# Kernel optimization log

Hardware: AMD Instinct MI355X
Metric: run time of the kernel (lower is better)

The kernel has to match this reference:

```python
import jax, jax.numpy as jnp
import numpy as np

DIM = 2048
H = 16
QLR = 1536
KVLR = 512
NOPE = 128
ROPE = 64
VH = 128
QKH = NOPE + ROPE  # 192
B, S = 2, 2048
EPS = 1e-6


def _rmsnorm(x, w):
    return x * jax.lax.rsqrt(jnp.mean(x * x, axis=-1, keepdims=True) + EPS) * w


def _rope_cos_sin(seq_len, r, dtype):
    inv_freq = 1.0 / (10000.0 ** (jnp.arange(0, r, 2, dtype=jnp.float32) / r))
    ang = jnp.arange(seq_len, dtype=jnp.float32)[:, None] * inv_freq  # [S, r/2]
    return jnp.cos(ang).astype(dtype), jnp.sin(ang).astype(dtype)


def _rot(t, cos, sin):
    # rotate-half RoPE on last dim; cos/sin pre-broadcast to t's rank
    t1, t2 = jnp.split(t, 2, axis=-1)
    return jnp.concatenate([t1 * cos - t2 * sin, t2 * cos + t1 * sin], axis=-1)


def setup_inputs() -> dict:
    key = jax.random.key(0)
    ks = jax.random.split(key, 12)
    sd = 0.02
    return {
        "x": jax.random.normal(ks[0], (B, S, DIM), jnp.float32),
        "wqd": jax.random.normal(ks[1], (DIM, QLR), jnp.float32) * sd,
        "bqd": jnp.zeros((QLR,), jnp.float32),
        "qnorm_w": jnp.ones((QLR,), jnp.float32),
        "wqu": jax.random.normal(ks[2], (QLR, H * QKH), jnp.float32) * sd,
        "bqu": jnp.zeros((H * QKH,), jnp.float32),
        "wkvd": jax.random.normal(ks[3], (DIM, KVLR + ROPE), jnp.float32) * sd,
        "bkvd": jnp.zeros((KVLR + ROPE,), jnp.float32),
        "kvnorm_w": jnp.ones((KVLR,), jnp.float32),
        "wkvu": jax.random.normal(ks[4], (KVLR, H * (NOPE + VH)), jnp.float32) * sd,
        "bkvu": jnp.zeros((H * (NOPE + VH),), jnp.float32),
        "wout": jax.random.normal(ks[5], (H * VH, DIM), jnp.float32) * sd,
        "bout": jnp.zeros((DIM,), jnp.float32),
    }


def reference(x, wqd, bqd, qnorm_w, wqu, bqu, wkvd, bkvd, kvnorm_w, wkvu, bkvu, wout, bout):
    b, s, _ = x.shape
    # Q path: low-rank down, RMSNorm, up; split nope / rope
    q = _rmsnorm(x @ wqd + bqd, qnorm_w) @ wqu + bqu        # [b,s,H*QKH]
    q = q.reshape(b, s, H, QKH)
    q_nope, q_rope = q[..., :NOPE], q[..., NOPE:]
    # KV path: joint down-proj -> kv latent + shared rope key
    kvd = x @ wkvd + bkvd                                   # [b,s,KVLR+ROPE]
    kv_lora, k_rope = kvd[..., :KVLR], kvd[..., KVLR:]
    cos, sin = _rope_cos_sin(s, ROPE, x.dtype)
    q_rope = _rot(q_rope, cos[None, :, None, :], sin[None, :, None, :])
    k_rope = _rot(k_rope, cos[None, :, :], sin[None, :, :])  # [b,s,ROPE]
    kvu = _rmsnorm(kv_lora, kvnorm_w) @ wkvu + bkvu          # [b,s,H*(NOPE+VH)]
    kvu = kvu.reshape(b, s, H, NOPE + VH)
    k_nope, v = kvu[..., :NOPE], kvu[..., NOPE:]
    k_rope_b = jnp.broadcast_to(k_rope[:, :, None, :], (b, s, H, ROPE))
    qf = jnp.concatenate([q_nope, q_rope], axis=-1)          # [b,s,H,QKH]
    kf = jnp.concatenate([k_nope, k_rope_b], axis=-1)        # [b,s,H,QKH]
    scale = QKH ** -0.5
    scores = jnp.einsum('bqhd,bkhd->bhqk', qf, kf) * scale
    causal = jnp.tril(jnp.ones((s, s), bool))
    scores = jnp.where(causal, scores, jnp.finfo(scores.dtype).min)
    attn = jax.nn.softmax(scores, axis=-1)
    o = jnp.einsum('bhqk,bkhd->bqhd', attn, v).reshape(b, s, H * VH)
    return o @ wout + bout
```

## Files before the change

kernel.cpp:

```cpp
#include <hip/hip_runtime.h>
#include <hip/hip_bf16.h>
#include <math.h>

#define HH 16
#define SS 2048
#define BBATCH 2
#define NROWS 4096

typedef __attribute__((ext_vector_type(8))) __bf16 bf16x8;
typedef __attribute__((ext_vector_type(4))) float f32x4;
typedef const __attribute__((address_space(1))) unsigned int* gas1_t;
typedef __attribute__((address_space(3))) unsigned int* las3_t;

__device__ __forceinline__ unsigned short f2bf(float f) {
  unsigned u = __builtin_bit_cast(unsigned, f);
  u += 0x7fffu + ((u >> 16) & 1u);
  return (unsigned short)(u >> 16);
}

__device__ __forceinline__ void gload16(const void* g, void* l) {
  __builtin_amdgcn_global_load_lds((gas1_t)g, (las3_t)l, 16, 0, 0);
}
__device__ __forceinline__ f32x4 mfma16(bf16x8 a, bf16x8 b, f32x4 c) {
  return __builtin_amdgcn_mfma_f32_16x16x32_bf16(a, b, c, 0, 0, 0);
}

__global__ __launch_bounds__(256) void k_convert(const float* __restrict__ in,
                                                 unsigned short* __restrict__ out, long n4) {
  long i = (long)blockIdx.x * blockDim.x + threadIdx.x;
  long stride = (long)gridDim.x * blockDim.x;
  for (; i < n4; i += stride) {
    float4 v = ((const float4*)in)[i];
    ushort4 o = { f2bf(v.x), f2bf(v.y), f2bf(v.z), f2bf(v.w) };
    ((ushort4*)out)[i] = o;
  }
}

__global__ __launch_bounds__(256) void k_transpose(const float* __restrict__ W,
                                                   unsigned short* __restrict__ Wt,
                                                   int K, int N, int Npad) {
  __shared__ float tile[32][33];
  int n0 = blockIdx.x * 32, k0 = blockIdx.y * 32;
  int tx = threadIdx.x & 31, ty = threadIdx.x >> 5;
  for (int i = ty; i < 32; i += 8) {
    int k = k0 + i, n = n0 + tx;
    tile[i][tx] = (k < K && n < N) ? W[(long)k * N + n] : 0.f;
  }
  __syncthreads();
  for (int i = ty; i < 32; i += 8) {
    int n = n0 + i, k = k0 + tx;
    if (n < Npad && k < K) Wt[(long)n * K + k] = f2bf(tile[tx][i]);
  }
}

__global__ __launch_bounds__(256) void k_bias_merge(const float* __restrict__ bqd,
                                                    const float* __restrict__ bkvd,
                                                    float* __restrict__ mb) {
  int i = blockIdx.x * 256 + threadIdx.x;
  if (i < 2176) mb[i] = i < 1536 ? bqd[i] : (i < 2112 ? bkvd[i - 1536] : 0.f);
}

__global__ __launch_bounds__(64) void k_rope_table(float2* __restrict__ tab) {
  int s = blockIdx.x * 2 + (threadIdx.x >> 5);
  int i = threadIdx.x & 31;
  float inv = powf(10000.f, -(float)i / 32.f);
  float ang = (float)s * inv;
  float sn, cs;
  sincosf(ang, &sn, &cs);
  tab[s * 32 + i] = make_float2(cs, sn);
}

__global__ __launch_bounds__(256) void k_gemm(const unsigned short* __restrict__ A,
                                              const unsigned short* __restrict__ Bt,
                                              const float* __restrict__ bias,
                                              float* __restrict__ C,
                                              int M, int N, int K) {
  __shared__ unsigned short lA[128 * 32];
  __shared__ unsigned short lB[128 * 32];
  int tid = threadIdx.x;
  int wave = tid >> 6, lane = tid & 63;
  int l15 = lane & 15, lhi = lane >> 4;
  int ntn = (N + 127) >> 7;
  int tm = blockIdx.x / ntn, tn = blockIdx.x % ntn;
  long row0 = (long)tm * 128, col0 = (long)tn * 128;
  int wr = wave >> 1, wc = wave & 1;

  const unsigned short* gA = A + (row0 + (tid >> 2)) * K + (tid & 3) * 8;
  const unsigned short* gB = Bt + (col0 + (tid >> 2)) * K + (tid & 3) * 8;
  unsigned short* lA0 = &lA[tid * 8];
  unsigned short* lB0 = &lB[tid * 8];

  f32x4 acc[4][4] = {};
  for (int k0 = 0; k0 < K; k0 += 32) {
    __syncthreads();
    gload16(gA + k0, lA0);
    gload16(gA + (long)64 * K + k0, lA0 + 2048);
    gload16(gB + k0, lB0);
    gload16(gB + (long)64 * K + k0, lB0 + 2048);
    asm volatile("s_waitcnt vmcnt(0)" ::: "memory");
    __syncthreads();
    bf16x8 af[4], bfr[4];
#pragma unroll
    for (int i = 0; i < 4; ++i) {
      af[i]  = *(const bf16x8*)&lA[(wr * 64 + i * 16 + l15) * 32 + lhi * 8];
      bfr[i] = *(const bf16x8*)&lB[(wc * 64 + i * 16 + l15) * 32 + lhi * 8];
    }
#pragma unroll
    for (int i = 0; i < 4; ++i)
#pragma unroll
      for (int j = 0; j < 4; ++j)
        acc[i][j] = mfma16(af[i], bfr[j], acc[i][j]);
  }
#pragma unroll
  for (int i = 0; i < 4; ++i)
#pragma unroll
    for (int j = 0; j < 4; ++j) {
      long r = row0 + wr * 64 + i * 16 + lhi * 4;
      long c = col0 + wc * 64 + j * 16 + l15;
      if (c < N) {
        float bv = bias[c];
#pragma unroll
        for (int rr = 0; rr < 4; ++rr)
          C[(r + rr) * N + c] = acc[i][j][rr] + bv;
      }
    }
}

__global__ __launch_bounds__(256) void k_gemm_qf(const unsigned short* __restrict__ A,
                                                 const unsigned short* __restrict__ Bt,
                                                 const float* __restrict__ bias,
                                                 const float2* __restrict__ rtab,
                                                 unsigned short* __restrict__ qf,
                                                 int M, int N, int K) {
  __shared__ unsigned short lA[128 * 32];
  __shared__ unsigned short lB[128 * 32];
  int tid = threadIdx.x;
  int wave = tid >> 6, lane = tid & 63;
  int l15 = lane & 15, lhi = lane >> 4;
  int ntn = (N + 127) >> 7;
  int tm = blockIdx.x / ntn, tn = blockIdx.x % ntn;
  long row0 = (long)tm * 128, col0 = (long)tn * 128;
  int wr = wave >> 1, wc = wave & 1;

  const unsigned short* gA = A + (row0 + (tid >> 2)) * K + (tid & 3) * 8;
  const unsigned short* gB = Bt + (col0 + (tid >> 2)) * K + (tid & 3) * 8;
  unsigned short* lA0 = &lA[tid * 8];
  unsigned short* lB0 = &lB[tid * 8];

  f32x4 acc[4][4] = {};
  for (int k0 = 0; k0 < K; k0 += 32) {
    __syncthreads();
    gload16(gA + k0, lA0);
    gload16(gA + (long)64 * K + k0, lA0 + 2048);
    gload16(gB + k0, lB0);
    gload16(gB + (long)64 * K + k0, lB0 + 2048);
    asm volatile("s_waitcnt vmcnt(0)" ::: "memory");
    __syncthreads();
    bf16x8 af[4], bfr[4];
#pragma unroll
    for (int i = 0; i < 4; ++i) {
      af[i]  = *(const bf16x8*)&lA[(wr * 64 + i * 16 + l15) * 32 + lhi * 8];
      bfr[i] = *(const bf16x8*)&lB[(wc * 64 + i * 16 + l15) * 32 + lhi * 8];
    }
#pragma unroll
    for (int i = 0; i < 4; ++i)
#pragma unroll
      for (int j = 0; j < 4; ++j)
        acc[i][j] = mfma16(af[i], bfr[j], acc[i][j]);
  }

  const float scq = 0.07216878364870322f * 1.4426950408889634f;
  int base = (int)col0 + wc * 64;
  int h = base / 192;
  int m192 = base - h * 192;
  float bv[4];
#pragma unroll
  for (int j = 0; j < 4; ++j) bv[j] = bias[base + j * 16 + l15];

#pragma unroll
  for (int i = 0; i < 4; ++i) {
#pragma unroll
    for (int rr = 0; rr < 4; ++rr) {
      long r = row0 + wr * 64 + i * 16 + lhi * 4 + rr;
      int s = (int)(r & 2047), b = (int)(r >> 11);
      unsigned short* dst = qf + (((long)(b * HH + h)) * SS + s) * 192;
      if (m192 < 128) {
#pragma unroll
        for (int j = 0; j < 4; ++j)
          dst[m192 + j * 16 + l15] = f2bf((acc[i][j][rr] + bv[j]) * scq);
      } else {
#pragma unroll
        for (int j = 0; j < 2; ++j) {
          int ifq = j * 16 + l15;
          float2 cs = rtab[s * 32 + ifq];
          float v1 = acc[i][j][rr] + bv[j];
          float v2 = acc[i][j + 2][rr] + bv[j + 2];
          dst[128 + ifq] = f2bf((v1 * cs.x - v2 * cs.y) * scq);
          dst[160 + ifq] = f2bf((v2 * cs.x + v1 * cs.y) * scq);
        }
      }
    }
  }
}

__global__ __launch_bounds__(256) void k_gemm_kv(const unsigned short* __restrict__ A,
                                                 const unsigned short* __restrict__ Bt,
                                                 const float* __restrict__ bias,
                                                 unsigned short* __restrict__ kf3,
                                                 unsigned short* __restrict__ vt3,
                                                 int M, int N, int K) {
  __shared__ unsigned short smem[16384];
  unsigned short* lA = smem;
  unsigned short* lB = smem + 4096;
  int tid = threadIdx.x;
  int wave = tid >> 6, lane = tid & 63;
  int l15 = lane & 15, lhi = lane >> 4;
  int ntn = N >> 7;
  int tm = blockIdx.x / ntn, tn = blockIdx.x % ntn;
  long row0 = (long)tm * 128, col0 = (long)tn * 128;
  int wr = wave >> 1, wc = wave & 1;

  const unsigned short* gA = A + (row0 + (tid >> 2)) * K + (tid & 3) * 8;
  const unsigned short* gB = Bt + (col0 + (tid >> 2)) * K + (tid & 3) * 8;
  unsigned short* lA0 = &lA[tid * 8];
  unsigned short* lB0 = &lB[tid * 8];

  f32x4 acc[4][4] = {};
  for (int k0 = 0; k0 < K; k0 += 32) {
    __syncthreads();
    gload16(gA + k0, lA0);
    gload16(gA + (long)64 * K + k0, lA0 + 2048);
    gload16(gB + k0, lB0);
    gload16(gB + (long)64 * K + k0, lB0 + 2048);
    asm volatile("s_waitcnt vmcnt(0)" ::: "memory");
    __syncthreads();
    bf16x8 af[4], bfr[4];
#pragma unroll
    for (int i = 0; i < 4; ++i) {
      af[i]  = *(const bf16x8*)&lA[(wr * 64 + i * 16 + l15) * 32 + lhi * 8];
      bfr[i] = *(const bf16x8*)&lB[(wc * 64 + i * 16 + l15) * 32 + lhi * 8];
    }
#pragma unroll
    for (int i = 0; i < 4; ++i)
#pragma unroll
      for (int j = 0; j < 4; ++j)
        acc[i][j] = mfma16(af[i], bfr[j], acc[i][j]);
  }

  int base = (int)col0 + wc * 64;
  int h = base >> 8;
  bool isv = (base & 255) >= 128;
  float bv[4];
#pragma unroll
  for (int j = 0; j < 4; ++j) bv[j] = bias[base + j * 16 + l15];

  int b = (int)(row0 >> 11);
  long bh = (long)b * HH + h;
  int lrb = wr * 64;
  __syncthreads();

  if (isv) {
#pragma unroll
    for (int i = 0; i < 4; ++i) {
      int lr = lrb + i * 16 + lhi * 4;
#pragma unroll
      for (int j = 0; j < 4; ++j) {
        int lc = wc * 64 + j * 16 + l15;
        ushort4 pk = { f2bf(acc[i][j][0] + bv[j]), f2bf(acc[i][j][1] + bv[j]),
                       f2bf(acc[i][j][2] + bv[j]), f2bf(acc[i][j][3] + bv[j]) };
        *(ushort4*)&smem[((lr >> 5) << 12) + lc * 32 + (lr & 31)] = pk;
      }
    }
    __syncthreads();
    long dst0 = (bh * 64 + ((row0 & 2047) >> 5)) * 4096;
#pragma unroll
    for (int p = 0; p < 8; ++p) {
      int e = p * 256 + tid;
      *(uint4*)&vt3[dst0 + e * 8] = *(uint4*)&smem[e * 8];
    }
  } else {
#pragma unroll
    for (int i = 0; i < 4; ++i) {
      int lr0 = lrb + i * 16 + lhi * 4;
#pragma unroll
      for (int j = 0; j < 4; ++j) {
        int c = (base & 255) + j * 16 + l15;
        int tbase = ((lr0 >> 4) << 11) + ((c >> 5) << 9) + (((c >> 3) & 3) << 7) + (c & 7);
#pragma unroll
        for (int rr = 0; rr < 4; ++rr)
          smem[tbase + ((lr0 + rr) & 15) * 8] = f2bf(acc[i][j][rr] + bv[j]);
      }
    }
    __syncthreads();
    long kb3 = (bh * 128 + ((row0 & 2047) >> 4)) * 3072;
#pragma unroll
    for (int p = 0; p < 8; ++p) {
      int e = p * 256 + tid;
      int tile = e >> 6;
      int off = (e & 63) * 8;
      long dst = kb3 + ((long)(tile >> 2) * 6 + (tile & 3)) * 512 + off;
      *(uint4*)&kf3[dst] = *(uint4*)&smem[tile * 512 + off];
    }
  }
}

__global__ __launch_bounds__(256) void k_rmsnorm(const float* __restrict__ X,
                                                 const float* __restrict__ w,
                                                 unsigned short* __restrict__ Y,
                                                 int L, int ldx) {
  long row = blockIdx.x;
  const float* x = X + row * ldx;
  float ss = 0.f;
  int n4 = L >> 2;
  for (int i = threadIdx.x; i < n4; i += 256) {
    float4 v = ((const float4*)x)[i];
    ss += v.x * v.x + v.y * v.y + v.z * v.z + v.w * v.w;
  }
  for (int off = 32; off > 0; off >>= 1) ss += __shfl_xor(ss, off);
  __shared__ float sb[4];
  if ((threadIdx.x & 63) == 0) sb[threadIdx.x >> 6] = ss;
  __syncthreads();
  float scale = rsqrtf((sb[0] + sb[1] + sb[2] + sb[3]) / (float)L + 1e-6f);
  unsigned short* y = Y + row * L;
  for (int i = threadIdx.x; i < L; i += 256)
    y[i] = f2bf(x[i] * scale * w[i]);
}

__global__ __launch_bounds__(64) void k_extract_krope(const float* __restrict__ sC,
                                                      unsigned short* __restrict__ kf3) {
  int bs = blockIdx.x;
  int lane = threadIdx.x;
  int s = bs & (SS - 1), b = bs >> 11;
  const float* src = sC + (long)bs * 2176 + 2048;
  int i = lane & 31;
  float inv = powf(10000.f, -(float)i / 32.f);
  float ang = (float)s * inv;
  float sn, cs;
  sincosf(ang, &sn, &cs);
  float t1 = src[i], t2 = src[32 + i];
  float v = (lane < 32) ? (t1 * cs - t2 * sn) : (t2 * cs + t1 * sn);
  unsigned short bv = f2bf(v);
  int d = 128 + lane;
  long inner = (long)(d >> 5) * 512 + ((d >> 3) & 3) * 128 + (s & 15) * 8 + (d & 7);
#pragma unroll
  for (int h = 0; h < HH; ++h) {
    long blk = ((long)(b * HH + h) * 128 + (s >> 4)) * 6;
    kf3[blk * 512 + inner] = bv;
  }
}

__global__ __launch_bounds__(256, 4) void k_attn(const unsigned short* __restrict__ qf,
                                                 const unsigned short* __restrict__ kf3,
                                                 const unsigned short* __restrict__ vt3,
                                                 unsigned short* __restrict__ o,
                                                 float* __restrict__ pO,
                                                 float* __restrict__ pml) {
  __shared__ unsigned short kbuf[64 * 192];
  __shared__ unsigned short pbuf[4][16 * 72];
  int tid = threadIdx.x;
  int wave = tid >> 6, lane = tid & 63;
  int l15 = lane & 15, lhi = lane >> 4;
  int idx = blockIdx.x;
  int rp = idx >> 5, bh = idx & 31;
  int qt, t0, t1, item;
  bool dodiag;
  if (rp < 48) {
    qt = 31 - (rp >> 1);
    int part = rp & 1;
    int h0 = (qt + 1) >> 1;
    t0 = part ? h0 : 0;
    t1 = part ? qt + 1 : h0;
    item = (bh * 24 + (qt - 8)) * 2 + part;
    dodiag = (part == 1);
  } else {
    qt = 55 - rp;
    t0 = 0;
    t1 = qt + 1;
    item = -1;
    dodiag = true;
  }
  int b = bh >> 4, h = bh & 15;
  int q0 = qt * 64;
  const char* kbase = (const char*)(kf3 + (long)bh * 128 * 3072);
  const unsigned short* vfrag0 = vt3 + (long)bh * 64 * 4096 + l15 * 32 + lhi * 8;
  const unsigned short* kread = kbuf + lane * 8;

  {
    const char* src = kbase + (long)t0 * 24576 + tid * 16;
    char* dst = (char*)kbuf + tid * 16;
#pragma unroll
    for (int p = 0; p < 6; ++p) gload16(src + p * 4096, dst + p * 4096);
  }

  const unsigned short* Qb = qf + ((long)bh * SS + q0 + wave * 16 + l15) * 192 + lhi * 8;
  bf16x8 qfr[6];
#pragma unroll
  for (int ks = 0; ks < 6; ++ks) qfr[ks] = *(const bf16x8*)(Qb + ks * 32);

  float m = -3e38f, ls = 0.f;
  f32x4 acc[8] = {};
  int qin = wave * 16 + l15;

  for (int t = t0; t < t1; ++t) {
    asm volatile("s_waitcnt vmcnt(0)" ::: "memory");
    __builtin_amdgcn_s_barrier();
    __builtin_amdgcn_sched_barrier(0);

    f32x4 sc[4] = {};
    __builtin_amdgcn_s_setprio(1);
#pragma unroll
    for (int ks = 0; ks < 6; ++ks) {
      bf16x8 kfr[4];
#pragma unroll
      for (int nf = 0; nf < 4; ++nf)
        kfr[nf] = *(const bf16x8*)&kread[(nf * 6 + ks) * 512];
#pragma unroll
      for (int nf = 0; nf < 4; ++nf)
        sc[nf] = mfma16(kfr[nf], qfr[ks], sc[nf]);
    }
    __builtin_amdgcn_s_setprio(0);
    __builtin_amdgcn_sched_barrier(0);
    __builtin_amdgcn_s_barrier();
    __builtin_amdgcn_sched_barrier(0);

    const unsigned short* vtb = vfrag0 + (long)t * 8192;
    bf16x8 v0[8];
#pragma unroll
    for (int nf = 0; nf < 8; ++nf) v0[nf] = *(const bf16x8*)(vtb + nf * 512);
    __builtin_amdgcn_sched_barrier(0);

    if (t + 1 < t1) {
      const char* src = kbase + (long)(t + 1) * 24576 + tid * 16;
      char* dst = (char*)kbuf + tid * 16;
#pragma unroll
      for (int p = 0; p < 6; ++p) gload16(src + p * 4096, dst + p * 4096);
    }

    bool diag = dodiag && (t == t1 - 1);
    float mnf[4];
#pragma unroll
    for (int nf = 0; nf < 4; ++nf) {
      if (diag) {
#pragma unroll
        for (int jj = 0; jj < 4; ++jj) {
          int kin = nf * 16 + lhi * 4 + jj;
          if (kin > qin) sc[nf][jj] = -3e38f;
        }
      }
      mnf[nf] = fmaxf(fmaxf(sc[nf][0], sc[nf][1]), fmaxf(sc[nf][2], sc[nf][3]));
    }
    float mx = fmaxf(fmaxf(mnf[0], mnf[1]), fmaxf(mnf[2], mnf[3]));
    mx = fmaxf(mx, __shfl_xor(mx, 16));
    mx = fmaxf(mx, __shfl_xor(mx, 32));
    if (!__all(mx <= m + 8.f)) {
      float mn = fmaxf(m, mx);
      float alpha = exp2f(m - mn);
      m = mn;
      ls *= alpha;
#pragma unroll
      for (int nf = 0; nf < 8; ++nf)
#pragma unroll
        for (int jj = 0; jj < 4; ++jj) acc[nf][jj] *= alpha;
    }
    float pnf[4];
#pragma unroll
    for (int nf = 0; nf < 4; ++nf) {
      float e0 = exp2f(sc[nf][0] - m), e1 = exp2f(sc[nf][1] - m);
      float e2 = exp2f(sc[nf][2] - m), e3 = exp2f(sc[nf][3] - m);
      pnf[nf] = (e0 + e1) + (e2 + e3);
      ushort4 pk = { f2bf(e0), f2bf(e1), f2bf(e2), f2bf(e3) };
      *(ushort4*)&pbuf[wave][l15 * 72 + nf * 16 + lhi * 4] = pk;
    }
    float ps = (pnf[0] + pnf[1]) + (pnf[2] + pnf[3]);
    ps += __shfl_xor(ps, 16);
    ps += __shfl_xor(ps, 32);
    ls += ps;

    {
      bf16x8 pf = *(const bf16x8*)&pbuf[wave][l15 * 72 + lhi * 8];
      __builtin_amdgcn_s_setprio(1);
#pragma unroll
      for (int nf = 0; nf < 8; ++nf) acc[nf] = mfma16(v0[nf], pf, acc[nf]);
      __builtin_amdgcn_s_setprio(0);
    }
    bf16x8 v1[8];
#pragma unroll
    for (int nf = 0; nf < 8; ++nf) v1[nf] = *(const bf16x8*)(vtb + 4096 + nf * 512);
    {
      bf16x8 pf = *(const bf16x8*)&pbuf[wave][l15 * 72 + 32 + lhi * 8];
      __builtin_amdgcn_s_setprio(1);
#pragma unroll
      for (int nf = 0; nf < 8; ++nf) acc[nf] = mfma16(v1[nf], pf, acc[nf]);
      __builtin_amdgcn_s_setprio(0);
    }
  }

  int qloc = wave * 16 + l15;
  if (item < 0) {
    float invl = 1.f / ls;
    long orow = (long)b * SS + q0 + qloc;
#pragma unroll
    for (int nf = 0; nf < 8; ++nf) {
      ushort4 ov = { f2bf(acc[nf][0] * invl), f2bf(acc[nf][1] * invl),
                     f2bf(acc[nf][2] * invl), f2bf(acc[nf][3] * invl) };
      *(ushort4*)&o[orow * 2048 + h * 128 + nf * 16 + lhi * 4] = ov;
    }
  } else {
    float* po = pO + (long)item * 8192 + qloc * 128;
#pragma unroll
    for (int nf = 0; nf < 8; ++nf)
      *(float4*)&po[nf * 16 + lhi * 4] = __builtin_bit_cast(float4, acc[nf]);
    if (lhi == 0) {
      pml[(long)item * 128 + qloc * 2] = m;
      pml[(long)item * 128 + qloc * 2 + 1] = ls;
    }
  }
}

__global__ __launch_bounds__(256) void k_merge(const float* __restrict__ pO,
                                               const float* __restrict__ pml,
                                               unsigned short* __restrict__ o) {
  int item2 = blockIdx.x;
  int bh = item2 / 24, qt = (item2 % 24) + 8;
  int b = bh >> 4, h = bh & 15;
  int q0 = qt * 64;
  long i0 = (long)item2 * 2, i1 = i0 + 1;
  __shared__ float w0s[64], w1s[64];
  int tid = threadIdx.x;
  if (tid < 64) {
    float m0 = pml[i0 * 128 + tid * 2], ls0 = pml[i0 * 128 + tid * 2 + 1];
    float m1 = pml[i1 * 128 + tid * 2], ls1 = pml[i1 * 128 + tid * 2 + 1];
    float mm = fmaxf(m0, m1);
    float w0 = exp2f(m0 - mm), w1 = exp2f(m1 - mm);
    float inv = 1.f / (ls0 * w0 + ls1 * w1);
    w0s[tid] = w0 * inv;
    w1s[tid] = w1 * inv;
  }
  __syncthreads();
  const float* p0 = pO + i0 * 8192;
  const float* p1 = pO + i1 * 8192;
#pragma unroll
  for (int p = 0; p < 8; ++p) {
    int e = p * 256 + tid;
    int q = e >> 5, d4 = (e & 31) * 4;
    float4 a = *(const float4*)&p0[q * 128 + d4];
    float4 c = *(const float4*)&p1[q * 128 + d4];
    float w0 = w0s[q], w1 = w1s[q];
    ushort4 ov = { f2bf(a.x * w0 + c.x * w1), f2bf(a.y * w0 + c.y * w1),
                   f2bf(a.z * w0 + c.z * w1), f2bf(a.w * w0 + c.w * w1) };
    *(ushort4*)&o[((long)b * SS + q0 + q) * 2048 + h * 128 + d4] = ov;
  }
}

extern "C" void kernel_launch(void* const* d_in, const int* in_sizes, int n_in,
                              void* d_out, int out_size, void* d_ws, size_t ws_size,
                              hipStream_t stream) {
  const float* x    = (const float*)d_in[0];
  const float* wqd  = (const float*)d_in[1];
  const float* bqd  = (const float*)d_in[2];
  const float* qnw  = (const float*)d_in[3];
  const float* wqu  = (const float*)d_in[4];
  const float* bqu  = (const float*)d_in[5];
  const float* wkvd = (const float*)d_in[6];
  const float* bkvd = (const float*)d_in[7];
  const float* kvnw = (const float*)d_in[8];
  const float* wkvu = (const float*)d_in[9];
  const float* bkvu = (const float*)d_in[10];
  const float* wout = (const float*)d_in[11];
  const float* bout = (const float*)d_in[12];
  float* out = (float*)d_out;

  char* ws = (char*)d_ws;
  size_t off = 0;
  auto alloc = [&](size_t sz) {
    char* p = ws + off;
    off += (sz + 255) & ~(size_t)255;
    return p;
  };
  unsigned short* xb    = (unsigned short*)alloc((size_t)NROWS * 2048 * 2);
  unsigned short* wqkt  = (unsigned short*)alloc((size_t)2176 * 2048 * 2);
  unsigned short* wqut  = (unsigned short*)alloc((size_t)3072 * 1536 * 2);
  unsigned short* wkvut = (unsigned short*)alloc((size_t)4096 * 512 * 2);
  unsigned short* woutt = (unsigned short*)alloc((size_t)2048 * 2048 * 2);
  unsigned short* qn    = (unsigned short*)alloc((size_t)NROWS * 1536 * 2);
  unsigned short* kvn   = (unsigned short*)alloc((size_t)NROWS * 512 * 2);
  unsigned short* qfb   = (unsigned short*)alloc((size_t)32 * SS * 192 * 2);
  unsigned short* kfb   = (unsigned short*)alloc((size_t)32 * SS * 192 * 2);
  unsigned short* vtb   = (unsigned short*)alloc((size_t)32 * 128 * SS * 2);
  unsigned short* ob    = (unsigned short*)alloc((size_t)NROWS * 2048 * 2);
  float*  mbias = (float*)alloc((size_t)2176 * 4);
  float2* rtab  = (float2*)alloc((size_t)SS * 32 * 8);
  float*  pO    = (float*)alloc((size_t)32 * 24 * 2 * 8192 * 4);
  float*  pml   = (float*)alloc((size_t)32 * 24 * 2 * 128 * 4);
  float* sC = (float*)alloc((size_t)NROWS * 2176 * 4);

  k_convert<<<2048, 256, 0, stream>>>(x, xb, (long)NROWS * 2048 / 4);
  k_transpose<<<dim3(48, 64), 256, 0, stream>>>(wqd, wqkt, 2048, 1536, 1536);
  k_transpose<<<dim3(20, 64), 256, 0, stream>>>(wkvd, wqkt + (size_t)1536 * 2048, 2048, 576, 640);
  k_transpose<<<dim3(96, 48), 256, 0, stream>>>(wqu, wqut, 1536, 3072, 3072);
  k_transpose<<<dim3(128, 16), 256, 0, stream>>>(wkvu, wkvut, 512, 4096, 4096);
  k_transpose<<<dim3(64, 64), 256, 0, stream>>>(wout, woutt, 2048, 2048, 2048);
  k_bias_merge<<<9, 256, 0, stream>>>(bqd, bkvd, mbias);
  k_rope_table<<<SS / 2, 64, 0, stream>>>(rtab);

  k_gemm<<<32 * 17, 256, 0, stream>>>(xb, wqkt, mbias, sC, NROWS, 2176, 2048);

  k_rmsnorm<<<NROWS, 256, 0, stream>>>(sC, qnw, qn, 1536, 2176);
  k_gemm_qf<<<32 * 24, 256, 0, stream>>>(qn, wqut, bqu, rtab, qfb, NROWS, 3072, 1536);

  k_rmsnorm<<<NROWS, 256, 0, stream>>>(sC + 1536, kvnw, kvn, 512, 2176);
  k_extract_krope<<<NROWS, 64, 0, stream>>>(sC, kfb);
  k_gemm_kv<<<32 * 32, 256, 0, stream>>>(kvn, wkvut, bkvu, kfb, vtb, NROWS, 4096, 512);

  k_attn<<<1792, 256, 0, stream>>>(qfb, kfb, vtb, ob, pO, pml);
  k_merge<<<768, 256, 0, stream>>>(pO, pml, ob);

  k_gemm<<<32 * 16, 256, 0, stream>>>(ob, woutt, bout, out, NROWS, 2048, 2048);
}
```

Before: 415.0 us.

## Split long causal attention rows into up to four KV parts; store down-proj in bf16

The attention work split changes from at most two KV chunks per query tile to two, three or four chunks depending on causal length, giving 2560 blocks in place of 1792. The merge kernel now combines up to four partial results with log-sum-exp weights. The goal is better load balance and fewer long tail blocks. Separately, the first down-projection GEMM now writes bf16 instead of fp32, which halves the traffic read by rmsnorm and the k_rope extract, at the cost of rounding the pre-norm activations to bf16.

```diff
diff --git a/kernel.cpp b/kernel.cpp
--- a/kernel.cpp
+++ b/kernel.cpp
@@ -16,6 +16,9 @@
   unsigned u = __builtin_bit_cast(unsigned, f);
   u += 0x7fffu + ((u >> 16) & 1u);
   return (unsigned short)(u >> 16);
+}
+__device__ __forceinline__ float bf2f(unsigned short u) {
+  return __builtin_bit_cast(float, (unsigned)u << 16);
 }
 
 __device__ __forceinline__ void gload16(const void* g, void* l) {
@@ -122,6 +125,62 @@
 #pragma unroll
         for (int rr = 0; rr < 4; ++rr)
           C[(r + rr) * N + c] = acc[i][j][rr] + bv;
+      }
+    }
+}
+
+__global__ __launch_bounds__(256) void k_gemm_c16(const unsigned short* __restrict__ A,
+                                                  const unsigned short* __restrict__ Bt,
+                                                  const float* __restrict__ bias,
+                                                  unsigned short* __restrict__ C,
+                                                  int M, int N, int K) {
+  __shared__ unsigned short lA[128 * 32];
+  __shared__ unsigned short lB[128 * 32];
+  int tid = threadIdx.x;
+  int wave = tid >> 6, lane = tid & 63;
+  int l15 = lane & 15, lhi = lane >> 4;
+  int ntn = (N + 127) >> 7;
+  int tm = blockIdx.x / ntn, tn = blockIdx.x % ntn;
+  long row0 = (long)tm * 128, col0 = (long)tn * 128;
+  int wr = wave >> 1, wc = wave & 1;
+
+  const unsigned short* gA = A + (row0 + (tid >> 2)) * K + (tid & 3) * 8;
+  const unsigned short* gB = Bt + (col0 + (tid >> 2)) * K + (tid & 3) * 8;
+  unsigned short* lA0 = &lA[tid * 8];
+  unsigned short* lB0 = &lB[tid * 8];
+
+  f32x4 acc[4][4] = {};
+  for (int k0 = 0; k0 < K; k0 += 32) {
+    __syncthreads();
+    gload16(gA + k0, lA0);
+    gload16(gA + (long)64 * K + k0, lA0 + 2048);
+    gload16(gB + k0, lB0);
+    gload16(gB + (long)64 * K + k0, lB0 + 2048);
+    asm volatile("s_waitcnt vmcnt(0)" ::: "memory");
+    __syncthreads();
+    bf16x8 af[4], bfr[4];
+#pragma unroll
+    for (int i = 0; i < 4; ++i) {
+      af[i]  = *(const bf16x8*)&lA[(wr * 64 + i * 16 + l15) * 32 + lhi * 8];
+      bfr[i] = *(const bf16x8*)&lB[(wc * 64 + i * 16 + l15) * 32 + lhi * 8];
+    }
+#pragma unroll
+    for (int i = 0; i < 4; ++i)
+#pragma unroll
+      for (int j = 0; j < 4; ++j)
+        acc[i][j] = mfma16(af[i], bfr[j], acc[i][j]);
+  }
+#pragma unroll
+  for (int i = 0; i < 4; ++i)
+#pragma unroll
+    for (int j = 0; j < 4; ++j) {
+      long r = row0 + wr * 64 + i * 16 + lhi * 4;
+      long c = col0 + wc * 64 + j * 16 + l15;
+      if (c < N) {
+        float bv = bias[c];
+#pragma unroll
+        for (int rr = 0; rr < 4; ++rr)
+          C[(r + rr) * N + c] = f2bf(acc[i][j][rr] + bv);
       }
     }
 }
@@ -304,17 +363,18 @@
   }
 }
 
-__global__ __launch_bounds__(256) void k_rmsnorm(const float* __restrict__ X,
+__global__ __launch_bounds__(256) void k_rmsnorm(const unsigned short* __restrict__ X,
                                                  const float* __restrict__ w,
                                                  unsigned short* __restrict__ Y,
                                                  int L, int ldx) {
   long row = blockIdx.x;
-  const float* x = X + row * ldx;
+  const unsigned short* x = X + row * ldx;
   float ss = 0.f;
   int n4 = L >> 2;
   for (int i = threadIdx.x; i < n4; i += 256) {
-    float4 v = ((const float4*)x)[i];
-    ss += v.x * v.x + v.y * v.y + v.z * v.z + v.w * v.w;
+    ushort4 v = ((const ushort4*)x)[i];
+    float a = bf2f(v.x), bb = bf2f(v.y), c = bf2f(v.z), d = bf2f(v.w);
+    ss += a * a + bb * bb + c * c + d * d;
   }
   for (int off = 32; off > 0; off >>= 1) ss += __shfl_xor(ss, off);
   __shared__ float sb[4];
@@ -323,21 +383,21 @@
   float scale = rsqrtf((sb[0] + sb[1] + sb[2] + sb[3]) / (float)L + 1e-6f);
   unsigned short* y = Y + row * L;
   for (int i = threadIdx.x; i < L; i += 256)
-    y[i] = f2bf(x[i] * scale * w[i]);
-}
-
-__global__ __launch_bounds__(64) void k_extract_krope(const float* __restrict__ sC,
+    y[i] = f2bf(bf2f(x[i]) * scale * w[i]);
+}
+
+__global__ __launch_bounds__(64) void k_extract_krope(const unsigned short* __restrict__ sC,
                                                       unsigned short* __restrict__ kf3) {
   int bs = blockIdx.x;
   int lane = threadIdx.x;
   int s = bs & (SS - 1), b = bs >> 11;
-  const float* src = sC + (long)bs * 2176 + 2048;
+  const unsigned short* src = sC + (long)bs * 2176 + 2048;
   int i = lane & 31;
   float inv = powf(10000.f, -(float)i / 32.f);
   float ang = (float)s * inv;
   float sn, cs;
   sincosf(ang, &sn, &cs);
-  float t1 = src[i], t2 = src[32 + i];
+  float t1 = bf2f(src[i]), t2 = bf2f(src[32 + i]);
   float v = (lane < 32) ? (t1 * cs - t2 * sn) : (t2 * cs + t1 * sn);
   unsigned short bv = f2bf(v);
   int d = 128 + lane;
@@ -362,22 +422,19 @@
   int l15 = lane & 15, lhi = lane >> 4;
   int idx = blockIdx.x;
   int rp = idx >> 5, bh = idx & 31;
-  int qt, t0, t1, item;
-  bool dodiag;
-  if (rp < 48) {
-    qt = 31 - (rp >> 1);
-    int part = rp & 1;
-    int h0 = (qt + 1) >> 1;
-    t0 = part ? h0 : 0;
-    t1 = part ? qt + 1 : h0;
-    item = (bh * 24 + (qt - 8)) * 2 + part;
-    dodiag = (part == 1);
-  } else {
-    qt = 55 - rp;
-    t0 = 0;
-    t1 = qt + 1;
-    item = -1;
-    dodiag = true;
+  int qt, part, np;
+  if (rp < 32)      { qt = 24 + (rp >> 2); part = rp & 3; np = 4; }
+  else if (rp < 56) { int r = rp - 32; qt = 16 + r / 3; part = r % 3; np = 3; }
+  else if (rp < 72) { int r = rp - 56; qt = 8 + (r >> 1); part = r & 1; np = 2; }
+  else              { qt = 79 - rp; part = 0; np = 1; }
+  int nt = qt + 1;
+  int t0 = nt * part / np, t1 = nt * (part + 1) / np;
+  bool dodiag = (part == np - 1);
+  int item;
+  if (np == 1) item = -1;
+  else {
+    int base = (qt < 16) ? (qt - 8) * 2 : (qt < 24) ? 16 + (qt - 16) * 3 : 40 + (qt - 24) * 4;
+    item = bh * 72 + base + part;
   }
   int b = bh >> 4, h = bh & 15;
   int q0 = qt * 64;
@@ -520,34 +577,45 @@
 __global__ __launch_bounds__(256) void k_merge(const float* __restrict__ pO,
                                                const float* __restrict__ pml,
                                                unsigned short* __restrict__ o) {
-  int item2 = blockIdx.x;
-  int bh = item2 / 24, qt = (item2 % 24) + 8;
+  int g = blockIdx.x;
+  int bh = g / 24, qt = (g % 24) + 8;
   int b = bh >> 4, h = bh & 15;
   int q0 = qt * 64;
-  long i0 = (long)item2 * 2, i1 = i0 + 1;
-  __shared__ float w0s[64], w1s[64];
+  int np = qt < 16 ? 2 : (qt < 24 ? 3 : 4);
+  int base = (qt < 16) ? (qt - 8) * 2 : (qt < 24) ? 16 + (qt - 16) * 3 : 40 + (qt - 24) * 4;
+  long i0 = (long)bh * 72 + base;
+  __shared__ float wts[4][64];
   int tid = threadIdx.x;
   if (tid < 64) {
-    float m0 = pml[i0 * 128 + tid * 2], ls0 = pml[i0 * 128 + tid * 2 + 1];
-    float m1 = pml[i1 * 128 + tid * 2], ls1 = pml[i1 * 128 + tid * 2 + 1];
-    float mm = fmaxf(m0, m1);
-    float w0 = exp2f(m0 - mm), w1 = exp2f(m1 - mm);
-    float inv = 1.f / (ls0 * w0 + ls1 * w1);
-    w0s[tid] = w0 * inv;
-    w1s[tid] = w1 * inv;
+    float mp0 = -3e38f, mp1 = -3e38f, mp2 = -3e38f, mp3 = -3e38f;
+    float lp0 = 0.f, lp1 = 0.f, lp2 = 0.f, lp3 = 0.f;
+    mp0 = pml[(i0 + 0) * 128 + tid * 2]; lp0 = pml[(i0 + 0) * 128 + tid * 2 + 1];
+    mp1 = pml[(i0 + 1) * 128 + tid * 2]; lp1 = pml[(i0 + 1) * 128 + tid * 2 + 1];
+    if (np > 2) { mp2 = pml[(i0 + 2) * 128 + tid * 2]; lp2 = pml[(i0 + 2) * 128 + tid * 2 + 1]; }
+    if (np > 3) { mp3 = pml[(i0 + 3) * 128 + tid * 2]; lp3 = pml[(i0 + 3) * 128 + tid * 2 + 1]; }
+    float mm = fmaxf(fmaxf(mp0, mp1), fmaxf(mp2, mp3));
+    float w0 = exp2f(mp0 - mm), w1 = exp2f(mp1 - mm);
+    float w2 = (np > 2) ? exp2f(mp2 - mm) : 0.f;
+    float w3 = (np > 3) ? exp2f(mp3 - mm) : 0.f;
+    float inv = 1.f / (lp0 * w0 + lp1 * w1 + lp2 * w2 + lp3 * w3);
+    wts[0][tid] = w0 * inv; wts[1][tid] = w1 * inv;
+    wts[2][tid] = w2 * inv; wts[3][tid] = w3 * inv;
   }
   __syncthreads();
-  const float* p0 = pO + i0 * 8192;
-  const float* p1 = pO + i1 * 8192;
-#pragma unroll
-  for (int p = 0; p < 8; ++p) {
-    int e = p * 256 + tid;
+#pragma unroll
+  for (int pp = 0; pp < 8; ++pp) {
+    int e = pp * 256 + tid;
     int q = e >> 5, d4 = (e & 31) * 4;
-    float4 a = *(const float4*)&p0[q * 128 + d4];
-    float4 c = *(const float4*)&p1[q * 128 + d4];
-    float w0 = w0s[q], w1 = w1s[q];
-    ushort4 ov = { f2bf(a.x * w0 + c.x * w1), f2bf(a.y * w0 + c.y * w1),
-                   f2bf(a.z * w0 + c.z * w1), f2bf(a.w * w0 + c.w * w1) };
+    float4 s = { 0.f, 0.f, 0.f, 0.f };
+#pragma unroll
+    for (int p = 0; p < 4; ++p) {
+      if (p < np) {
+        float4 a = *(const float4*)&pO[(i0 + p) * 8192 + q * 128 + d4];
+        float w = wts[p][q];
+        s.x += a.x * w; s.y += a.y * w; s.z += a.z * w; s.w += a.w * w;
+      }
+    }
+    ushort4 ov = { f2bf(s.x), f2bf(s.y), f2bf(s.z), f2bf(s.w) };
     *(ushort4*)&o[((long)b * SS + q0 + q) * 2048 + h * 128 + d4] = ov;
   }
 }
@@ -590,9 +658,9 @@
   unsigned short* ob    = (unsigned short*)alloc((size_t)NROWS * 2048 * 2);
   float*  mbias = (float*)alloc((size_t)2176 * 4);
   float2* rtab  = (float2*)alloc((size_t)SS * 32 * 8);
-  float*  pO    = (float*)alloc((size_t)32 * 24 * 2 * 8192 * 4);
-  float*  pml   = (float*)alloc((size_t)32 * 24 * 2 * 128 * 4);
-  float* sC = (float*)alloc((size_t)NROWS * 2176 * 4);
+  float*  pO    = (float*)alloc((size_t)2304 * 8192 * 4);
+  float*  pml   = (float*)alloc((size_t)2304 * 128 * 4);
+  unsigned short* sCb = (unsigned short*)alloc((size_t)NROWS * 2176 * 2);
 
   k_convert<<<2048, 256, 0, stream>>>(x, xb, (long)NROWS * 2048 / 4);
   k_transpose<<<dim3(48, 64), 256, 0, stream>>>(wqd, wqkt, 2048, 1536, 1536);
@@ -603,16 +671,16 @@
   k_bias_merge<<<9, 256, 0, stream>>>(bqd, bkvd, mbias);
   k_rope_table<<<SS / 2, 64, 0, stream>>>(rtab);
 
-  k_gemm<<<32 * 17, 256, 0, stream>>>(xb, wqkt, mbias, sC, NROWS, 2176, 2048);
-
-  k_rmsnorm<<<NROWS, 256, 0, stream>>>(sC, qnw, qn, 1536, 2176);
+  k_gemm_c16<<<32 * 17, 256, 0, stream>>>(xb, wqkt, mbias, sCb, NROWS, 2176, 2048);
+
+  k_rmsnorm<<<NROWS, 256, 0, stream>>>(sCb, qnw, qn, 1536, 2176);
   k_gemm_qf<<<32 * 24, 256, 0, stream>>>(qn, wqut, bqu, rtab, qfb, NROWS, 3072, 1536);
 
-  k_rmsnorm<<<NROWS, 256, 0, stream>>>(sC + 1536, kvnw, kvn, 512, 2176);
-  k_extract_krope<<<NROWS, 64, 0, stream>>>(sC, kfb);
+  k_rmsnorm<<<NROWS, 256, 0, stream>>>(sCb + 1536, kvnw, kvn, 512, 2176);
+  k_extract_krope<<<NROWS, 64, 0, stream>>>(sCb, kfb);
   k_gemm_kv<<<32 * 32, 256, 0, stream>>>(kvn, wkvut, bkvu, kfb, vtb, NROWS, 4096, 512);
 
-  k_attn<<<1792, 256, 0, stream>>>(qfb, kfb, vtb, ob, pO, pml);
+  k_attn<<<2560, 256, 0, stream>>>(qfb, kfb, vtb, ob, pO, pml);
   k_merge<<<768, 256, 0, stream>>>(pO, pml, ob);
 
   k_gemm<<<32 * 16, 256, 0, stream>>>(ob, woutt, bout, out, NROWS, 2048, 2048);
```

Measured after the change: 414.9 us. No clear change (-0.0%).
